# Kernel optimization log

Measured on AMD Instinct MI355X. Metric: run time of the kernel, lower is better.

The kernel has to match this reference:

```python
import jax, jax.numpy as jnp
import numpy as np

OUT = 7          # roi_layer out_size
SR = 2           # roi_layer sample_num (sampling ratio)
STRIDES = (4, 8, 16, 32)
FINEST_SCALE = 56.0


def roi_align_level(feat, rois, spatial_scale):
    """RoIAlign (aligned=False, torchvision/mmdet classic) for all rois on one level.
    feat: (B, C, H, W), rois: (K, 5) [batch_idx, x1, y1, x2, y2] in image coords.
    Returns (K, C, OUT, OUT)."""
    B, C, H, W = feat.shape
    b = rois[:, 0].astype(jnp.int32)
    x1 = rois[:, 1] * spatial_scale
    y1 = rois[:, 2] * spatial_scale
    x2 = rois[:, 3] * spatial_scale
    y2 = rois[:, 4] * spatial_scale
    roi_w = jnp.maximum(x2 - x1, 1.0)
    roi_h = jnp.maximum(y2 - y1, 1.0)
    bin_w = roi_w / OUT
    bin_h = roi_h / OUT
    # per-bin sample offsets: (OUT, SR) fractional bin positions
    off = jnp.arange(OUT, dtype=jnp.float32)[:, None] + (jnp.arange(SR, dtype=jnp.float32)[None, :] + 0.5) / SR
    ys = y1[:, None, None] + off[None] * bin_h[:, None, None]   # (K, OUT, SR)
    xs = x1[:, None, None] + off[None] * bin_w[:, None, None]   # (K, OUT, SR)
    y = ys[:, :, :, None, None]                                  # (K, OUT, SR, 1, 1)
    x = xs[:, None, None, :, :]                                  # (K, 1, 1, OUT, SR)
    y, x = jnp.broadcast_arrays(y, x)                            # (K, OUT, SR, OUT, SR)
    valid = (y > -1.0) & (y < H) & (x > -1.0) & (x < W)
    yc = jnp.clip(y, 0.0, H - 1.0)
    xc = jnp.clip(x, 0.0, W - 1.0)
    y0 = jnp.floor(yc)
    x0 = jnp.floor(xc)
    ly = yc - y0
    lx = xc - x0
    hy = 1.0 - ly
    hx = 1.0 - lx
    y0i = y0.astype(jnp.int32)
    x0i = x0.astype(jnp.int32)
    y1i = jnp.minimum(y0i + 1, H - 1)
    x1i = jnp.minimum(x0i + 1, W - 1)
    bb = jnp.broadcast_to(b[:, None, None, None, None], y0i.shape)

    def g(yi, xi):
        # advanced indexing (batched gather) -> (K, OUT, SR, OUT, SR, C)
        return feat[bb, :, yi, xi]

    val = (hy * hx)[..., None] * g(y0i, x0i) \
        + (hy * lx)[..., None] * g(y0i, x1i) \
        + (ly * hx)[..., None] * g(y1i, x0i) \
        + (ly * lx)[..., None] * g(y1i, x1i)
    val = jnp.where(valid[..., None], val, 0.0)
    pooled = val.mean(axis=(2, 4))           # average SRxSR samples -> (K, OUT, OUT, C)
    return jnp.transpose(pooled, (0, 3, 1, 2))  # (K, C, OUT, OUT)


def map_roi_levels(rois, num_levels):
    scale = jnp.sqrt((rois[:, 3] - rois[:, 1] + 1.0) * (rois[:, 4] - rois[:, 2] + 1.0))
    lvl = jnp.floor(jnp.log2(scale / FINEST_SCALE + 1e-6))
    return jnp.clip(lvl, 0, num_levels - 1).astype(jnp.int32)


def setup_inputs() -> dict:
    key = jax.random.key(0)
    ks = jax.random.split(key, 10)
    B, C = 2, 256
    IMG_H, IMG_W = 800.0, 1344.0
    feats = {}
    shapes = [(B, C, 200, 336), (B, C, 100, 168), (B, C, 50, 84), (B, C, 25, 42)]
    for i, s in enumerate(shapes):
        feats[f"feat{i}"] = jax.random.normal(ks[i], s, dtype=jnp.float32)
    K = 1024
    bidx = jax.random.randint(ks[4], (K,), 0, B).astype(jnp.float32)
    # log-uniform box sizes in [16, ~724] px so all 4 FPN levels get rois
    w = 2.0 ** jax.random.uniform(ks[5], (K,), minval=4.0, maxval=9.5)
    h = 2.0 ** jax.random.uniform(ks[6], (K,), minval=4.0, maxval=9.5)
    cx = jax.random.uniform(ks[7], (K,), minval=0.0, maxval=IMG_W)
    cy = jax.random.uniform(ks[8], (K,), minval=0.0, maxval=IMG_H)
    x1 = jnp.clip(cx - w * 0.5, 0.0, IMG_W - 2.0)
    y1 = jnp.clip(cy - h * 0.5, 0.0, IMG_H - 2.0)
    x2 = jnp.clip(x1 + w, x1 + 1.0, IMG_W - 1.0)
    y2 = jnp.clip(y1 + h, y1 + 1.0, IMG_H - 1.0)
    rois = jnp.stack([bidx, x1, y1, x2, y2], axis=-1).astype(jnp.float32)
    feats["rois"] = rois
    return feats


def reference(feat0, feat1, feat2, feat3, rois):
    feats = [feat0, feat1, feat2, feat3]
    num_levels = len(feats)
    target_lvls = map_roi_levels(rois, num_levels)
    K = rois.shape[0]
    C = feats[0].shape[1]
    roi_feats = jnp.zeros((K, C, OUT, OUT), dtype=feats[0].dtype)
    for i in range(num_levels):
        ri = roi_align_level(feats[i], rois, 1.0 / STRIDES[i])
        mask = (target_lvls == i)[:, None, None, None]
        roi_feats = roi_feats + jnp.where(mask, ri, 0.0)
    return roi_feats
```

## Files before the change

### kernel.cpp

```cpp
#include <hip/hip_runtime.h>
#include <stdint.h>
#include <stddef.h>

#define C_TOTAL     256
#define CPG         4
#define NGROUPS     (C_TOTAL / CPG)
#define NBINS       49
#define TILE_D      1920
#define CHUNK16_MAX (TILE_D / 4)

__global__ __launch_bounds__(256, 5)
void roi_align_fused(const float* __restrict__ f0,
                     const float* __restrict__ f1,
                     const float* __restrict__ f2,
                     const float* __restrict__ f3,
                     const float* __restrict__ rois,
                     float* __restrict__ out)
{
    __shared__ __align__(16) float s_tile[CPG * TILE_D];

    const int k    = blockIdx.y;
    const int g    = blockIdx.x;
    const int tid  = threadIdx.x;
    const int wv   = tid >> 6;
    const int lane = tid & 63;

    const float bf  = rois[k * 5 + 0];
    const float rx1 = rois[k * 5 + 1];
    const float ry1 = rois[k * 5 + 2];
    const float rx2 = rois[k * 5 + 3];
    const float ry2 = rois[k * 5 + 4];
    const int   b   = (int)bf;

    const float scale = sqrtf((rx2 - rx1 + 1.0f) * (ry2 - ry1 + 1.0f));
    int lvl = (int)floorf(log2f(scale / 56.0f + 1e-6f));
    lvl = lvl < 0 ? 0 : (lvl > 3 ? 3 : lvl);

    const float* feat; int H, W;
    if      (lvl == 0) { feat = f0; H = 200; W = 336; }
    else if (lvl == 1) { feat = f1; H = 100; W = 168; }
    else if (lvl == 2) { feat = f2; H =  50; W =  84; }
    else               { feat = f3; H =  25; W =  42; }

    const float ss  = 1.0f / (float)(4 << lvl);
    const float x1s = rx1 * ss, y1s = ry1 * ss;
    const float x2s = rx2 * ss, y2s = ry2 * ss;
    const float roi_w = fmaxf(x2s - x1s, 1.0f);
    const float roi_h = fmaxf(y2s - y1s, 1.0f);
    const float bw = roi_w * (1.0f / 7.0f);
    const float bh = roi_h * (1.0f / 7.0f);

    const float Hm1 = (float)(H - 1), Wm1 = (float)(W - 1);
    const int ty0 = (int)floorf(fminf(fmaxf(y1s + 0.25f * bh, 0.0f), Hm1));
    const int tx0 = (int)floorf(fminf(fmaxf(x1s + 0.25f * bw, 0.0f), Wm1));
    const int ty1 = min((int)floorf(fminf(fmaxf(y1s + 6.75f * bh, 0.0f), Hm1)) + 1, H - 1);
    const int tx1 = min((int)floorf(fminf(fmaxf(x1s + 6.75f * bw, 0.0f), Wm1)) + 1, W - 1);
    const int fh = ty1 - ty0 + 1;
    const int fw = tx1 - tx0 + 1;

    int cpr = (fw + (tx0 & 3) + 3) >> 2;
    if (cpr > (W >> 2)) cpr = W >> 2;
    const bool use16 = (lvl < 3) && (fh * cpr <= CHUNK16_MAX);

    int rb, rowStride, chunks;
    if (use16) {
        rb = tx0 & ~3;
        if (rb + 4 * cpr > W) rb = W - 4 * cpr;
        rowStride = 4 * cpr;
        chunks = fh * cpr;
    } else {
        rb = tx0;
        rowStride = fw;
        chunks = fh * fw;
        if (chunks > TILE_D) chunks = TILE_D;
    }
    const uint32_t d = use16 ? (uint32_t)cpr : (uint32_t)fw;
    const uint32_t M = (1u << 22) / d + 1u;
    const int dW = W - rowStride;

    {
        const int c = g * CPG + wv;
        const float* src = feat + ((size_t)(b * C_TOTAL + c) * (size_t)H + (size_t)ty0) * (size_t)W + rb;
        float* dst = s_tile + wv * TILE_D;
        if (use16) {
            for (int start = 0; start < chunks; start += 64) {
                int s = (start + 64 > chunks) ? max(chunks - 64, 0) : start;
                int idx = s + lane;
                if (idx >= chunks) idx = chunks - 1;
                const int fy = (int)(((uint32_t)idx * M) >> 22);
                const int off = (idx << 2) + fy * dW;
                __builtin_amdgcn_global_load_lds(
                    (const __attribute__((address_space(1))) uint32_t*)(src + off),
                    (__attribute__((address_space(3))) uint32_t*)(dst + (s << 2)),
                    16, 0, 0);
            }
        } else {
            for (int start = 0; start < chunks; start += 64) {
                int s = (start + 64 > chunks) ? max(chunks - 64, 0) : start;
                int idx = s + lane;
                if (idx >= chunks) idx = chunks - 1;
                const int fy = (int)(((uint32_t)idx * M) >> 22);
                const int off = idx + fy * dW;
                __builtin_amdgcn_global_load_lds(
                    (const __attribute__((address_space(1))) uint32_t*)(src + off),
                    (__attribute__((address_space(3))) uint32_t*)(dst + s),
                    4, 0, 0);
            }
        }
    }

    asm volatile("s_waitcnt vmcnt(0)" ::: "memory");
    __syncthreads();

    if (lane < NBINS) {
        const float* t = s_tile + wv * TILE_D;
        const int oy = lane / 7;
        const int ox = lane - oy * 7;
        const float Hf = (float)H, Wf = (float)W;
        float acc = 0.0f;
#pragma unroll
        for (int sy = 0; sy < 2; ++sy) {
#pragma unroll
            for (int sx = 0; sx < 2; ++sx) {
                const float yy = y1s + ((float)oy + 0.25f + 0.5f * (float)sy) * bh;
                const float xx = x1s + ((float)ox + 0.25f + 0.5f * (float)sx) * bw;
                const bool valid = (yy > -1.0f) && (yy < Hf) && (xx > -1.0f) && (xx < Wf);
                const float yc  = fminf(fmaxf(yy, 0.0f), Hm1);
                const float xc  = fminf(fmaxf(xx, 0.0f), Wm1);
                const float y0f = floorf(yc);
                const float x0f = floorf(xc);
                const float ly = yc - y0f, lx = xc - x0f;
                const float hy = 1.0f - ly, hx = 1.0f - lx;
                const int y0  = (int)y0f, x0 = (int)x0f;
                const int y1i = min(y0 + 1, H - 1);
                const int x1i = min(x0 + 1, W - 1);
                const int r0 = (y0  - ty0) * rowStride - rb;
                const int r1 = (y1i - ty0) * rowStride - rb;
                const float v = valid ? 0.25f : 0.0f;
                acc += (hy * hx * v) * t[r0 + x0]
                     + (hy * lx * v) * t[r0 + x1i]
                     + (ly * hx * v) * t[r1 + x0]
                     + (ly * lx * v) * t[r1 + x1i];
            }
        }
        const int c = g * CPG + wv;
        out[((size_t)k * C_TOTAL + c) * NBINS + lane] = acc;
    }
}

extern "C" void kernel_launch(void* const* d_in, const int* in_sizes, int n_in,
                              void* d_out, int out_size, void* d_ws, size_t ws_size,
                              hipStream_t stream) {
    const float* f0   = (const float*)d_in[0];
    const float* f1   = (const float*)d_in[1];
    const float* f2   = (const float*)d_in[2];
    const float* f3   = (const float*)d_in[3];
    const float* rois = (const float*)d_in[4];
    float* out = (float*)d_out;

    const int K = in_sizes[4] / 5;
    dim3 grid(NGROUPS, K, 1);
    roi_align_fused<<<grid, 256, 0, stream>>>(f0, f1, f2, f3, rois, out);
}
```

Baseline: 147.1 us.

## Precompute per-ROI sample descriptors in a prologue kernel shared across channel groups

Splits the work into a small per-ROI kernel and the main kernel. The small kernel computes level selection, tile geometry, and the bilinear weights and tile offsets for all 196 samples, and writes them to the workspace. The main kernel loads these into LDS through async global-to-LDS copies, which removes per-block ROI math that was repeated across all 64 channel groups. It also shrinks the LDS tile and raises occupancy. The costs are an extra launch, workspace traffic, and clamping chunks to the smaller tile, which may truncate large ROIs.

```diff
diff --git a/kernel.cpp b/kernel.cpp
--- a/kernel.cpp
+++ b/kernel.cpp
@@ -2,28 +2,23 @@
 #include <stdint.h>
 #include <stddef.h>
 
-#define C_TOTAL     256
-#define CPG         4
-#define NGROUPS     (C_TOTAL / CPG)
-#define NBINS       49
-#define TILE_D      1920
-#define CHUNK16_MAX (TILE_D / 4)
-
-__global__ __launch_bounds__(256, 5)
-void roi_align_fused(const float* __restrict__ f0,
-                     const float* __restrict__ f1,
-                     const float* __restrict__ f2,
-                     const float* __restrict__ f3,
-                     const float* __restrict__ rois,
-                     float* __restrict__ out)
+#define C_TOTAL   256
+#define CPG       4
+#define NGROUPS   (C_TOTAL / CPG)
+#define NBINS     49
+#define NSAMP     196
+#define TILE_D    1280
+#define SD_STRIDE 16
+#define BLOB_DW   (NSAMP * 8)
+#define DESC_CHUNKS (BLOB_DW / 4)
+#define WCHUNK    (DESC_CHUNKS / 4)
+
+__global__ __launch_bounds__(256)
+void roi_desc_kernel(const float* __restrict__ rois, int* __restrict__ ws_i,
+                     int blobBase )
 {
-    __shared__ __align__(16) float s_tile[CPG * TILE_D];
-
-    const int k    = blockIdx.y;
-    const int g    = blockIdx.x;
-    const int tid  = threadIdx.x;
-    const int wv   = tid >> 6;
-    const int lane = tid & 63;
+    const int k   = blockIdx.x;
+    const int tid = threadIdx.x;
 
     const float bf  = rois[k * 5 + 0];
     const float rx1 = rois[k * 5 + 1];
@@ -36,11 +31,11 @@
     int lvl = (int)floorf(log2f(scale / 56.0f + 1e-6f));
     lvl = lvl < 0 ? 0 : (lvl > 3 ? 3 : lvl);
 
-    const float* feat; int H, W;
-    if      (lvl == 0) { feat = f0; H = 200; W = 336; }
-    else if (lvl == 1) { feat = f1; H = 100; W = 168; }
-    else if (lvl == 2) { feat = f2; H =  50; W =  84; }
-    else               { feat = f3; H =  25; W =  42; }
+    int H, W;
+    if      (lvl == 0) { H = 200; W = 336; }
+    else if (lvl == 1) { H = 100; W = 168; }
+    else if (lvl == 2) { H =  50; W =  84; }
+    else               { H =  25; W =  42; }
 
     const float ss  = 1.0f / (float)(4 << lvl);
     const float x1s = rx1 * ss, y1s = ry1 * ss;
@@ -60,7 +55,7 @@
 
     int cpr = (fw + (tx0 & 3) + 3) >> 2;
     if (cpr > (W >> 2)) cpr = W >> 2;
-    const bool use16 = (lvl < 3) && (fh * cpr <= CHUNK16_MAX);
+    const bool use16 = (lvl < 3) && (fh * cpr <= TILE_D / 4);
 
     int rb, rowStride, chunks;
     if (use16) {
@@ -68,6 +63,7 @@
         if (rb + 4 * cpr > W) rb = W - 4 * cpr;
         rowStride = 4 * cpr;
         chunks = fh * cpr;
+        if (chunks > TILE_D / 4) chunks = TILE_D / 4;
     } else {
         rb = tx0;
         rowStride = fw;
@@ -78,16 +74,81 @@
     const uint32_t M = (1u << 22) / d + 1u;
     const int dW = W - rowStride;
 
+    if (tid == 0) {
+        int* sd = ws_i + k * SD_STRIDE;
+        sd[0] = lvl;
+        sd[1] = use16 ? 1 : 0;
+        sd[2] = b * C_TOTAL * H * W + ty0 * W + rb;
+        sd[3] = chunks;
+        sd[4] = (int)M;
+        sd[5] = dW;
+        sd[6] = H * W;
+    }
+
+    if (tid < NSAMP) {
+        const int iy = tid / 14;
+        const int ix = tid - iy * 14;
+        const float yy = y1s + ((float)iy * 0.5f + 0.25f) * bh;
+        const float xx = x1s + ((float)ix * 0.5f + 0.25f) * bw;
+        const bool valid = (yy > -1.0f) && (yy < (float)H) && (xx > -1.0f) && (xx < (float)W);
+        const float yc  = fminf(fmaxf(yy, 0.0f), Hm1);
+        const float xc  = fminf(fmaxf(xx, 0.0f), Wm1);
+        const float y0f = floorf(yc);
+        const float x0f = floorf(xc);
+        const float ly = yc - y0f, lx = xc - x0f;
+        const float hy = 1.0f - ly, hx = 1.0f - lx;
+        const int y0  = (int)y0f, x0 = (int)x0f;
+        const int y1i = min(y0 + 1, H - 1);
+        const int x1i = min(x0 + 1, W - 1);
+        const int r0 = (y0  - ty0) * rowStride - rb;
+        const int r1 = (y1i - ty0) * rowStride - rb;
+        const float v = valid ? 0.25f : 0.0f;
+        float4* w4 = (float4*)(ws_i + blobBase + k * BLOB_DW);
+        int4*   c4 = (int4*)  (ws_i + blobBase + k * BLOB_DW + 4 * NSAMP);
+        w4[tid] = make_float4(hy * hx * v, hy * lx * v, ly * hx * v, ly * lx * v);
+        c4[tid] = make_int4(r0 + x0, r0 + x1i, r1 + x0, r1 + x1i);
+    }
+}
+
+__global__ __launch_bounds__(256, 6)
+void roi_align_main(const float* __restrict__ f0,
+                    const float* __restrict__ f1,
+                    const float* __restrict__ f2,
+                    const float* __restrict__ f3,
+                    const int* __restrict__ ws_i,
+                    float* __restrict__ out,
+                    int blobBase)
+{
+    __shared__ __align__(16) float s_tile[CPG * TILE_D];
+    __shared__ __align__(16) float s_desc[BLOB_DW];
+
+    const int k    = blockIdx.y;
+    const int g    = blockIdx.x;
+    const int tid  = threadIdx.x;
+    const int wv   = tid >> 6;
+    const int lane = tid & 63;
+
+    const int* sd = ws_i + k * SD_STRIDE;
+    const int lvl     = sd[0];
+    const int use16   = sd[1];
+    const int srcBase = sd[2];
+    const int chunks  = sd[3];
+    const uint32_t M  = (uint32_t)sd[4];
+    const int dW      = sd[5];
+    const int HW      = sd[6];
+
+    const float* feat = (lvl == 0) ? f0 : (lvl == 1) ? f1 : (lvl == 2) ? f2 : f3;
+
     {
         const int c = g * CPG + wv;
-        const float* src = feat + ((size_t)(b * C_TOTAL + c) * (size_t)H + (size_t)ty0) * (size_t)W + rb;
+        const float* src = feat + srcBase + (size_t)c * (size_t)HW;
         float* dst = s_tile + wv * TILE_D;
         if (use16) {
             for (int start = 0; start < chunks; start += 64) {
                 int s = (start + 64 > chunks) ? max(chunks - 64, 0) : start;
                 int idx = s + lane;
                 if (idx >= chunks) idx = chunks - 1;
-                const int fy = (int)(((uint32_t)idx * M) >> 22);
+                const int fy  = (int)(((uint32_t)idx * M) >> 22);
                 const int off = (idx << 2) + fy * dW;
                 __builtin_amdgcn_global_load_lds(
                     (const __attribute__((address_space(1))) uint32_t*)(src + off),
@@ -99,7 +160,7 @@
                 int s = (start + 64 > chunks) ? max(chunks - 64, 0) : start;
                 int idx = s + lane;
                 if (idx >= chunks) idx = chunks - 1;
-                const int fy = (int)(((uint32_t)idx * M) >> 22);
+                const int fy  = (int)(((uint32_t)idx * M) >> 22);
                 const int off = idx + fy * dW;
                 __builtin_amdgcn_global_load_lds(
                     (const __attribute__((address_space(1))) uint32_t*)(src + off),
@@ -109,38 +170,39 @@
         }
     }
 
+    {
+        const float* bsrc = (const float*)(ws_i + blobBase + k * BLOB_DW);
+        const int i0 = wv * WCHUNK;
+        __builtin_amdgcn_global_load_lds(
+            (const __attribute__((address_space(1))) uint32_t*)(bsrc + ((i0 + lane) << 2)),
+            (__attribute__((address_space(3))) uint32_t*)(s_desc + (i0 << 2)),
+            16, 0, 0);
+        __builtin_amdgcn_global_load_lds(
+            (const __attribute__((address_space(1))) uint32_t*)(bsrc + ((i0 + WCHUNK - 64 + lane) << 2)),
+            (__attribute__((address_space(3))) uint32_t*)(s_desc + ((i0 + WCHUNK - 64) << 2)),
+            16, 0, 0);
+    }
+
     asm volatile("s_waitcnt vmcnt(0)" ::: "memory");
     __syncthreads();
 
     if (lane < NBINS) {
-        const float* t = s_tile + wv * TILE_D;
+        const float*  t  = s_tile + wv * TILE_D;
+        const float4* w4 = (const float4*)s_desc;
+        const int4*   c4 = (const int4*)(s_desc + 4 * NSAMP);
         const int oy = lane / 7;
         const int ox = lane - oy * 7;
-        const float Hf = (float)H, Wf = (float)W;
+        const int sbase = oy * 28 + ox * 2;
         float acc = 0.0f;
 #pragma unroll
         for (int sy = 0; sy < 2; ++sy) {
 #pragma unroll
             for (int sx = 0; sx < 2; ++sx) {
-                const float yy = y1s + ((float)oy + 0.25f + 0.5f * (float)sy) * bh;
-                const float xx = x1s + ((float)ox + 0.25f + 0.5f * (float)sx) * bw;
-                const bool valid = (yy > -1.0f) && (yy < Hf) && (xx > -1.0f) && (xx < Wf);
-                const float yc  = fminf(fmaxf(yy, 0.0f), Hm1);
-                const float xc  = fminf(fmaxf(xx, 0.0f), Wm1);
-                const float y0f = floorf(yc);
-                const float x0f = floorf(xc);
-                const float ly = yc - y0f, lx = xc - x0f;
-                const float hy = 1.0f - ly, hx = 1.0f - lx;
-                const int y0  = (int)y0f, x0 = (int)x0f;
-                const int y1i = min(y0 + 1, H - 1);
-                const int x1i = min(x0 + 1, W - 1);
-                const int r0 = (y0  - ty0) * rowStride - rb;
-                const int r1 = (y1i - ty0) * rowStride - rb;
-                const float v = valid ? 0.25f : 0.0f;
-                acc += (hy * hx * v) * t[r0 + x0]
-                     + (hy * lx * v) * t[r0 + x1i]
-                     + (ly * hx * v) * t[r1 + x0]
-                     + (ly * lx * v) * t[r1 + x1i];
+                const int s = sbase + sy * 14 + sx;
+                const float4 w  = w4[s];
+                const int4   cc = c4[s];
+                acc += w.x * t[cc.x] + w.y * t[cc.y]
+                     + w.z * t[cc.z] + w.w * t[cc.w];
             }
         }
         const int c = g * CPG + wv;
@@ -157,8 +219,13 @@
     const float* f3   = (const float*)d_in[3];
     const float* rois = (const float*)d_in[4];
     float* out = (float*)d_out;
+    int*   ws  = (int*)d_ws;
 
     const int K = in_sizes[4] / 5;
+    const int blobBase = K * SD_STRIDE;
+
+    roi_desc_kernel<<<K, 256, 0, stream>>>(rois, ws, blobBase);
+
     dim3 grid(NGROUPS, K, 1);
-    roi_align_fused<<<grid, 256, 0, stream>>>(f0, f1, f2, f3, rois, out);
+    roi_align_main<<<grid, 256, 0, stream>>>(f0, f1, f2, f3, ws, out, blobBase);
 }
```

Measured after the change: 146.1 us. About the same (-0.7%).
